# Kernel optimization log

Measured on AMD Instinct MI355X. Metric: run time of the kernel, lower is better.

The kernel has to match this reference:

```python
import jax, jax.numpy as jnp
import numpy as np

D = 1024; H = 8; QLR = 384; KVLR = 256; NOPE = 128; ROPE = 64; VD = 128
E = 8; TOPK = 2; INTER = 512; NSH = 2; B = 2; T = 2048
QKD = NOPE + ROPE  # 192


def _rms(x, w, eps=1e-6):
    return x * jax.lax.rsqrt(jnp.mean(x * x, axis=-1, keepdims=True) + eps) * w


def _rope(x, cos, sin):
    # x: [B,T,h,ROPE]; pairs are consecutive elements (torch view(...,-1,2)).
    x0 = x[..., 0::2]
    x1 = x[..., 1::2]
    c = cos[None, :, None, :]
    s = sin[None, :, None, :]
    y0 = x0 * c - x1 * s
    y1 = x0 * s + x1 * c
    return jnp.stack([y0, y1], axis=-1).reshape(x.shape)


def setup_inputs() -> dict:
    key = jax.random.key(0)
    ks = jax.random.split(key, 12)
    def w(k, shape, scale=0.02):
        return jax.random.normal(k, shape, dtype=jnp.float32) * scale
    inv = 1.0 / (10000.0 ** (jnp.arange(0, ROPE, 2, dtype=jnp.float32) / ROPE))
    ang = jnp.arange(T, dtype=jnp.float32)[:, None] * inv[None, :]  # [T, ROPE//2]
    return {
        "x": jax.random.normal(ks[0], (B, T, D), dtype=jnp.float32),
        "freqs_cos": jnp.cos(ang),
        "freqs_sin": jnp.sin(ang),
        "rmsn1_w": jnp.ones((D,), jnp.float32),
        "rmsn2_w": jnp.ones((D,), jnp.float32),
        "latent_w": w(ks[1], (D, QLR + KVLR + ROPE)),
        "q_norm_w": jnp.ones((QLR,), jnp.float32),
        "q_up_w": w(ks[2], (QLR, H * QKD)),
        "kv_norm_w": jnp.ones((KVLR,), jnp.float32),
        "kv_up_w": w(ks[3], (KVLR, H * (NOPE + VD))),
        "c_proj_w": w(ks[4], (D, D)),
        "gate_w": w(ks[5], (D, E)),
        "sh_w1": w(ks[6], (D, INTER * NSH)),
        "sh_w2": w(ks[7], (INTER * NSH, D)),
        "sh_w3": w(ks[8], (D, INTER * NSH)),
        "e_w1": w(ks[9], (E, D, INTER)),
        "e_w2": w(ks[10], (E, INTER, D)),
        "e_w3": w(ks[11], (E, D, INTER)),
    }


def reference(x, freqs_cos, freqs_sin, rmsn1_w, rmsn2_w, latent_w, q_norm_w,
              q_up_w, kv_norm_w, kv_up_w, c_proj_w, gate_w, sh_w1, sh_w2,
              sh_w3, e_w1, e_w2, e_w3):
    Bx, Tx, _ = x.shape
    # ---- MLA attention ----
    h = _rms(x, rmsn1_w)
    lat = h @ latent_w
    q_l, kv_l, k_r = jnp.split(lat, [QLR, QLR + KVLR], axis=-1)
    q = (_rms(q_l, q_norm_w) @ q_up_w).reshape(Bx, Tx, H, QKD)
    q_n, q_r = q[..., :NOPE], q[..., NOPE:]
    q_r = _rope(q_r, freqs_cos, freqs_sin)
    q = jnp.concatenate([q_n, q_r], axis=-1)  # [B,T,H,QKD]
    kv = (_rms(kv_l, kv_norm_w) @ kv_up_w).reshape(Bx, Tx, H, NOPE + VD)
    k_n, v = kv[..., :NOPE], kv[..., NOPE:]
    k_r = _rope(k_r[:, :, None, :], freqs_cos, freqs_sin)
    k_r = jnp.broadcast_to(k_r, (Bx, Tx, H, ROPE))
    k = jnp.concatenate([k_n, k_r], axis=-1)
    scale = 1.0 / jnp.sqrt(jnp.float32(QKD))
    scores = jnp.einsum('bqhd,bkhd->bhqk', q, k) * scale
    causal = jnp.tril(jnp.ones((Tx, Tx), dtype=bool))
    scores = jnp.where(causal, scores, jnp.finfo(scores.dtype).min)
    attn = jax.nn.softmax(scores, axis=-1)
    y = jnp.einsum('bhqk,bkhd->bqhd', attn, v).reshape(Bx, Tx, D)
    x = x + y @ c_proj_w
    # ---- DeepSeekMoE ----
    h2 = _rms(x, rmsn2_w).reshape(-1, D)  # [N, D]
    y_sh = (jax.nn.silu(h2 @ sh_w1) * (h2 @ sh_w3)) @ sh_w2
    scores_g = jax.nn.softmax(h2 @ gate_w, axis=-1)  # [N, E]
    w_top, idx = jax.lax.top_k(scores_g, TOPK)  # weights == gathered original scores
    # combine weights per expert (route_scale = 1.0)
    cw = jnp.sum(jax.nn.one_hot(idx, E, dtype=h2.dtype) * w_top[..., None], axis=1)  # [N, E]
    h1 = jnp.einsum('nd,edi->eni', h2, e_w1)
    h3 = jnp.einsum('nd,edi->eni', h2, e_w3)
    out_e = jnp.einsum('eni,eid->end', jax.nn.silu(h1) * h3, e_w2)  # [E, N, D]
    y_moe = y_sh + jnp.einsum('end,ne->nd', out_e, cw)
    return x + y_moe.reshape(Bx, Tx, D)
```

## Files before the change

kernel.cpp:

```cpp
#include <hip/hip_runtime.h>
#include <hip/hip_bf16.h>
#include <math.h>

#define D_ 1024
#define H_ 8
#define QLR_ 384
#define KVLR_ 256
#define NOPE_ 128
#define ROPE_ 64
#define VD_ 128
#define E_ 8
#define INTER_ 512
#define B_ 2
#define T_ 2048
#define QKD_ 192
#define NTOK (B_*T_)
#define LSTR 4608
#define MAXMB 72
#define NCH 40

typedef __attribute__((ext_vector_type(8))) short short8;
typedef __attribute__((ext_vector_type(4))) float f32x4;
typedef __attribute__((ext_vector_type(4))) unsigned short us4;

__device__ __forceinline__ unsigned short f2bf(float f) {
  union { float f; unsigned u; } v; v.f = f;
  return (unsigned short)((v.u + 0x7FFFu + ((v.u >> 16) & 1u)) >> 16);
}
__device__ __forceinline__ float bf2f(unsigned short h) {
  union { unsigned u; float f; } v; v.u = ((unsigned)h) << 16;
  return v.f;
}

#define GLD16(SRC, DST) __builtin_amdgcn_global_load_lds( \
    (__attribute__((address_space(1))) void*)(SRC), \
    (__attribute__((address_space(3))) void*)(DST), 16, 0, 0)

#define DPPF(v, ctrl) __int_as_float(__builtin_amdgcn_update_dpp(0, __float_as_int(v), ctrl, 0xF, 0xF, true))
__device__ __forceinline__ float dppmax16(float v) {
  v = fmaxf(v, DPPF(v, 0xB1));
  v = fmaxf(v, DPPF(v, 0x4E));
  v = fmaxf(v, DPPF(v, 0x124));
  v = fmaxf(v, DPPF(v, 0x128));
  return v;
}
__device__ __forceinline__ float dppsum16(float v) {
  v += DPPF(v, 0xB1);
  v += DPPF(v, 0x4E);
  v += DPPF(v, 0x124);
  v += DPPF(v, 0x128);
  return v;
}

__device__ __forceinline__ void trans32(const float* __restrict__ src, unsigned short* __restrict__ dst,
                                        int R, int C, int c0, int r0, float (*tile)[33]) {
  int tx = threadIdx.x & 31, ty = threadIdx.x >> 5;
  #pragma unroll
  for (int i = 0; i < 4; ++i) {
    int rr = ty + i * 8;
    tile[rr][tx] = src[(size_t)(r0 + rr) * C + c0 + tx];
  }
  __syncthreads();
  #pragma unroll
  for (int i = 0; i < 4; ++i) {
    int rr = ty + i * 8;
    dst[(size_t)(c0 + rr) * R + r0 + tx] = f2bf(tile[tx][rr]);
  }
}
__device__ __forceinline__ void trans32p(const float* __restrict__ src, unsigned short* __restrict__ dst,
                                         int K, int C1, int c0, int r0, int f, float (*tile)[33]) {
  int tx = threadIdx.x & 31, ty = threadIdx.x >> 5;
  #pragma unroll
  for (int i = 0; i < 4; ++i) {
    int rr = ty + i * 8;
    tile[rr][tx] = src[(size_t)(r0 + rr) * C1 + c0 + tx];
  }
  __syncthreads();
  #pragma unroll
  for (int i = 0; i < 4; ++i) {
    int cc = ty + i * 8;
    int c = c0 + cc;
    int n = ((c >> 4) << 5) + (c & 15) + f;
    dst[(size_t)n * K + r0 + tx] = f2bf(tile[tx][cc]);
  }
}

__global__ __launch_bounds__(256) void prep1(
    const float* __restrict__ x, const float* __restrict__ rw, unsigned short* __restrict__ h_bf,
    const float* __restrict__ latent_w, unsigned short* __restrict__ Wlat) {
  __shared__ float tile[32][33];
  int b = blockIdx.x;
  if (b < NTOK) {
    int tid = threadIdx.x;
    const float* xr = x + (size_t)b * D_;
    float v[4]; float ss = 0.f;
    #pragma unroll
    for (int j = 0; j < 4; ++j) { v[j] = xr[tid + j * 256]; ss += v[j] * v[j]; }
    for (int o = 1; o < 64; o <<= 1) ss += __shfl_xor(ss, o);
    if ((tid & 63) == 0) tile[32][tid >> 6] = ss;
    __syncthreads();
    float inv = 1.f / sqrtf((tile[32][0] + tile[32][1] + tile[32][2] + tile[32][3]) / D_ + 1e-6f);
    #pragma unroll
    for (int j = 0; j < 4; ++j) {
      int i = tid + j * 256;
      h_bf[(size_t)b * D_ + i] = f2bf(v[j] * inv * rw[i]);
    }
    return;
  }
  b -= NTOK;
  trans32(latent_w, Wlat, 1024, 704, (b % 22) * 32, (b / 22) * 32, tile);
}

__global__ __launch_bounds__(256) void prep2(
    const unsigned short* __restrict__ h_bf, const unsigned short* __restrict__ Wlat,
    unsigned short* __restrict__ lat,
    const float* __restrict__ q_up_w, unsigned short* __restrict__ Wqup,
    const float* __restrict__ kv_up_w, unsigned short* __restrict__ Wkv,
    const float* __restrict__ c_proj_w, unsigned short* __restrict__ Wcp,
    const float* __restrict__ sh_w1, const float* __restrict__ sh_w3, unsigned short* __restrict__ Wsh13,
    const float* __restrict__ sh_w2, unsigned short* __restrict__ Wsh2,
    const float* __restrict__ e_w1, const float* __restrict__ e_w3, unsigned short* __restrict__ Wew13,
    const float* __restrict__ e_w2, unsigned short* __restrict__ Wew2) {
  __shared__ __align__(16) unsigned short As[128 * 32];
  __shared__ __align__(16) unsigned short Bs[128 * 32];
  __shared__ float tile[32][33];
  int b = blockIdx.x;
  if (b < 192) {
    const int tid = threadIdx.x, lane = tid & 63, wave = tid >> 6;
    const int wm = wave >> 1, wn = wave & 1;
    const int bm = (b / 6) * 128, bn = (b % 6) * 128;
    const int r = lane & 15, g = lane >> 4;
    f32x4 acc[4][4];
    #pragma unroll
    for (int i = 0; i < 4; ++i)
      #pragma unroll
      for (int j = 0; j < 4; ++j) acc[i][j] = (f32x4)0.f;
    const int rl0 = wave * 16 + (lane >> 2), rl1 = rl0 + 64;
    const int kc = (lane & 3) * 8;
    char* AsB = (char*)As; char* BsB = (char*)Bs;
    for (int k0 = 0; k0 < 1024; k0 += 32) {
      GLD16(h_bf + (size_t)(bm + rl0) * 1024 + k0 + kc, AsB + wave * 1024);
      GLD16(h_bf + (size_t)(bm + rl1) * 1024 + k0 + kc, AsB + (wave + 4) * 1024);
      GLD16(Wlat + (size_t)(bn + rl0) * 1024 + k0 + kc, BsB + wave * 1024);
      GLD16(Wlat + (size_t)(bn + rl1) * 1024 + k0 + kc, BsB + (wave + 4) * 1024);
      __syncthreads();
      short8 af[4], bfr[4];
      #pragma unroll
      for (int mi = 0; mi < 4; ++mi)
        af[mi] = *(const short8*)(As + (wm * 64 + mi * 16 + r) * 32 + g * 8);
      #pragma unroll
      for (int nj = 0; nj < 4; ++nj)
        bfr[nj] = *(const short8*)(Bs + (wn * 64 + nj * 16 + r) * 32 + g * 8);
      #pragma unroll
      for (int mi = 0; mi < 4; ++mi)
        #pragma unroll
        for (int nj = 0; nj < 4; ++nj)
          acc[mi][nj] = __builtin_amdgcn_mfma_f32_16x16x32_bf16(af[mi], bfr[nj], acc[mi][nj], 0, 0, 0);
      __syncthreads();
    }
    const int orow0 = wm * 64 + g * 4;
    const int ocol0 = bn + wn * 64 + r;
    #pragma unroll
    for (int mi = 0; mi < 4; ++mi)
      #pragma unroll
      for (int reg = 0; reg < 4; ++reg) {
        int mrow = bm + orow0 + mi * 16 + reg;
        size_t bas = (size_t)mrow * 768 + ocol0;
        #pragma unroll
        for (int nj = 0; nj < 4; ++nj) lat[bas + nj * 16] = f2bf(acc[mi][nj][reg]);
      }
    return;
  }
  b -= 192;
  if (b < 576) { trans32(q_up_w, Wqup, 384, 1536, (b % 48) * 32, (b / 48) * 32, tile); return; }
  b -= 576;
  if (b < 512) { trans32(kv_up_w, Wkv, 256, 2048, (b % 64) * 32, (b / 64) * 32, tile); return; }
  b -= 512;
  if (b < 1024) { trans32(c_proj_w, Wcp, 1024, 1024, (b % 32) * 32, (b / 32) * 32, tile); return; }
  b -= 1024;
  if (b < 1024) { trans32(sh_w2, Wsh2, 1024, 1024, (b % 32) * 32, (b / 32) * 32, tile); return; }
  b -= 1024;
  if (b < 2048) {
    int z = b / 1024, idx = b % 1024;
    trans32p(z ? sh_w3 : sh_w1, Wsh13, 1024, 1024, (idx % 32) * 32, (idx / 32) * 32, z * 16, tile);
    return;
  }
  b -= 2048;
  if (b < 8192) {
    int z = b / 512, idx = b % 512;
    int bat = z >> 1, f = (z & 1) * 16;
    const float* src = ((z & 1) ? e_w3 : e_w1) + (size_t)bat * 1024 * 512;
    trans32p(src, Wew13 + (size_t)bat * 1024 * 1024, 1024, 512, (idx % 16) * 32, (idx / 16) * 32, f, tile);
    return;
  }
  b -= 8192;
  {
    int z = b / 512, idx = b % 512;
    trans32(e_w2 + (size_t)z * 512 * 1024, Wew2 + (size_t)z * 1024 * 512,
            512, 1024, (idx % 32) * 32, (idx / 32) * 32, tile);
  }
}

__global__ __launch_bounds__(256) void lat_post(
    const unsigned short* __restrict__ lat, const float* __restrict__ qw,
    const float* __restrict__ kw, const float* __restrict__ fc, const float* __restrict__ fs,
    unsigned short* __restrict__ qn, unsigned short* __restrict__ kvn,
    unsigned short* __restrict__ kr) {
  int row = blockIdx.x, tid = threadIdx.x;
  int lane = tid & 63, wv = tid >> 6;
  const unsigned short* lr = lat + (size_t)row * 768;
  float s1 = 0.f, s2 = 0.f;
  for (int i = tid; i < QLR_; i += 256) { float v = bf2f(lr[i]); s1 += v * v; }
  { float v = bf2f(lr[QLR_ + tid]); s2 = v * v; }
  for (int o = 1; o < 64; o <<= 1) { s1 += __shfl_xor(s1, o); s2 += __shfl_xor(s2, o); }
  __shared__ float red[8];
  if (lane == 0) { red[wv] = s1; red[4 + wv] = s2; }
  __syncthreads();
  float inv1 = 1.f / sqrtf((red[0] + red[1] + red[2] + red[3]) / QLR_ + 1e-6f);
  float inv2 = 1.f / sqrtf((red[4] + red[5] + red[6] + red[7]) / KVLR_ + 1e-6f);
  for (int i = tid; i < QLR_; i += 256)
    qn[(size_t)row * QLR_ + i] = f2bf(bf2f(lr[i]) * inv1 * qw[i]);
  kvn[(size_t)row * KVLR_ + tid] = f2bf(bf2f(lr[QLR_ + tid]) * inv2 * kw[tid]);
  if (tid < 32) {
    int t = row & (T_ - 1);
    float c = fc[t * 32 + tid], s = fs[t * 32 + tid];
    float x0 = bf2f(lr[640 + 2 * tid]), x1 = bf2f(lr[640 + 2 * tid + 1]);
    kr[(size_t)row * ROPE_ + 2 * tid]     = f2bf(x0 * c - x1 * s);
    kr[(size_t)row * ROPE_ + 2 * tid + 1] = f2bf(x0 * s + x1 * c);
  }
}

template<int MODE>
__global__ __launch_bounds__(256) void gemm_bf16(
    const unsigned short* __restrict__ A, const unsigned short* __restrict__ Bt,
    void* __restrict__ Cv, int M, int N, int K,
    const float* __restrict__ addv) {
  __shared__ __align__(16) unsigned short As[128 * 32];
  __shared__ __align__(16) unsigned short Bs[128 * 32];
  const int tid = threadIdx.x;
  const int lane = tid & 63, wave = tid >> 6;
  const int wm = wave >> 1, wn = wave & 1;
  const int bm = blockIdx.y * 128, bn = blockIdx.x * 128;
  const int r = lane & 15, g = lane >> 4;

  f32x4 acc[4][4];
  #pragma unroll
  for (int i = 0; i < 4; ++i)
    #pragma unroll
    for (int j = 0; j < 4; ++j) acc[i][j] = (f32x4)0.f;

  const int rl0 = wave * 16 + (lane >> 2);
  const int rl1 = rl0 + 64;
  const int kc = (lane & 3) * 8;
  char* AsB = (char*)As; char* BsB = (char*)Bs;

  for (int k0 = 0; k0 < K; k0 += 32) {
    GLD16(A + (size_t)(bm + rl0) * K + k0 + kc, AsB + wave * 1024);
    GLD16(A + (size_t)(bm + rl1) * K + k0 + kc, AsB + (wave + 4) * 1024);
    GLD16(Bt + (size_t)(bn + rl0) * K + k0 + kc, BsB + wave * 1024);
    GLD16(Bt + (size_t)(bn + rl1) * K + k0 + kc, BsB + (wave + 4) * 1024);
    __syncthreads();
    short8 af[4], bfr[4];
    #pragma unroll
    for (int mi = 0; mi < 4; ++mi)
      af[mi] = *(const short8*)(As + (wm * 64 + mi * 16 + r) * 32 + g * 8);
    #pragma unroll
    for (int nj = 0; nj < 4; ++nj)
      bfr[nj] = *(const short8*)(Bs + (wn * 64 + nj * 16 + r) * 32 + g * 8);
    #pragma unroll
    for (int mi = 0; mi < 4; ++mi)
      #pragma unroll
      for (int nj = 0; nj < 4; ++nj)
        acc[mi][nj] = __builtin_amdgcn_mfma_f32_16x16x32_bf16(af[mi], bfr[nj], acc[mi][nj], 0, 0, 0);
    __syncthreads();
  }

  const int orow0 = wm * 64 + g * 4;
  const int ocol0 = bn + wn * 64 + r;
  #pragma unroll
  for (int mi = 0; mi < 4; ++mi) {
    #pragma unroll
    for (int reg = 0; reg < 4; ++reg) {
      int mrow = bm + orow0 + mi * 16 + reg;
      size_t bas = (size_t)mrow * N + ocol0;
      if (MODE == 0) {
        unsigned short* C = (unsigned short*)Cv;
        #pragma unroll
        for (int nj = 0; nj < 4; ++nj) C[bas + nj * 16] = f2bf(acc[mi][nj][reg]);
      } else {
        float* C = (float*)Cv;
        #pragma unroll
        for (int nj = 0; nj < 4; ++nj) C[bas + nj * 16] = acc[mi][nj][reg] + addv[bas + nj * 16];
      }
    }
  }
}

__global__ __launch_bounds__(256) void gemm_qkv(
    const unsigned short* __restrict__ qn, const unsigned short* __restrict__ Wqup,
    const unsigned short* __restrict__ kvn, const unsigned short* __restrict__ Wkv,
    unsigned short* __restrict__ qq, unsigned short* __restrict__ kvb,
    unsigned short* __restrict__ vtg) {
  __shared__ __align__(16) unsigned short As[128 * 32];
  __shared__ __align__(16) unsigned short Bs[128 * 32];
  const int tid = threadIdx.x;
  const int lane = tid & 63, wave = tid >> 6;
  const int wm = wave >> 1, wn = wave & 1;
  const bool isQ = blockIdx.x < 12;
  const int bx = isQ ? blockIdx.x : blockIdx.x - 12;
  const unsigned short* A  = isQ ? qn : kvn;
  const unsigned short* Bt = isQ ? Wqup : Wkv;
  const int K = isQ ? QLR_ : KVLR_;
  const int bm = blockIdx.y * 128, bn = bx * 128;
  const int r = lane & 15, g = lane >> 4;

  f32x4 acc[4][4];
  #pragma unroll
  for (int i = 0; i < 4; ++i)
    #pragma unroll
    for (int j = 0; j < 4; ++j) acc[i][j] = (f32x4)0.f;

  const int rl0 = wave * 16 + (lane >> 2);
  const int rl1 = rl0 + 64;
  const int kc = (lane & 3) * 8;
  char* AsB = (char*)As; char* BsB = (char*)Bs;

  for (int k0 = 0; k0 < K; k0 += 32) {
    GLD16(A + (size_t)(bm + rl0) * K + k0 + kc, AsB + wave * 1024);
    GLD16(A + (size_t)(bm + rl1) * K + k0 + kc, AsB + (wave + 4) * 1024);
    GLD16(Bt + (size_t)(bn + rl0) * K + k0 + kc, BsB + wave * 1024);
    GLD16(Bt + (size_t)(bn + rl1) * K + k0 + kc, BsB + (wave + 4) * 1024);
    __syncthreads();
    short8 af[4], bfr[4];
    #pragma unroll
    for (int mi = 0; mi < 4; ++mi)
      af[mi] = *(const short8*)(As + (wm * 64 + mi * 16 + r) * 32 + g * 8);
    #pragma unroll
    for (int nj = 0; nj < 4; ++nj)
      bfr[nj] = *(const short8*)(Bs + (wn * 64 + nj * 16 + r) * 32 + g * 8);
    #pragma unroll
    for (int mi = 0; mi < 4; ++mi)
      #pragma unroll
      for (int nj = 0; nj < 4; ++nj)
        acc[mi][nj] = __builtin_amdgcn_mfma_f32_16x16x32_bf16(af[mi], bfr[nj], acc[mi][nj], 0, 0, 0);
    __syncthreads();
  }

  if (isQ) {
// ... 176 lines not shown

  for (int k0 = 0; k0 < K; k0 += 32) {
    GLD16(A + (size_t)(bm + rl0) * K + k0 + kc, AsB + wave * 1024);
    GLD16(A + (size_t)(bm + rl1) * K + k0 + kc, AsB + (wave + 4) * 1024);
    GLD16(Bt + (size_t)(bn + rl0) * K + k0 + kc, BsB + wave * 1024);
    GLD16(Bt + (size_t)(bn + rl1) * K + k0 + kc, BsB + (wave + 4) * 1024);
    __syncthreads();
    short8 af[4], bfr[4];
    #pragma unroll
    for (int mi = 0; mi < 4; ++mi)
      af[mi] = *(const short8*)(As + (wm * 64 + mi * 16 + r) * 32 + g * 8);
    #pragma unroll
    for (int nj = 0; nj < 4; ++nj)
      bfr[nj] = *(const short8*)(Bs + (wn * 64 + nj * 16 + r) * 32 + g * 8);
    #pragma unroll
    for (int mi = 0; mi < 4; ++mi)
      #pragma unroll
      for (int nj = 0; nj < 4; ++nj)
        acc[mi][nj] = __builtin_amdgcn_mfma_f32_16x16x32_bf16(af[mi], bfr[nj], acc[mi][nj], 0, 0, 0);
    __syncthreads();
  }

  const int ocol0 = bn + wn * 64 + r;
  if (isSh) {
    #pragma unroll
    for (int mi = 0; mi < 4; ++mi)
      #pragma unroll
      for (int reg = 0; reg < 4; ++reg) {
        int mrow = bm + wm * 64 + mi * 16 + g * 4 + reg;
        #pragma unroll
        for (int nj = 0; nj < 4; ++nj)
          atomicAdd(out + (size_t)mrow * 1024 + ocol0 + nj * 16, acc[mi][nj][reg]);
      }
  } else {
    #pragma unroll
    for (int mi = 0; mi < 4; ++mi)
      #pragma unroll
      for (int reg = 0; reg < 4; ++reg) {
        int orow = wm * 64 + mi * 16 + g * 4 + reg;
        int tok = lists[e * LSTR + ib * 128 + orow];
        if (tok >= 0) {
          float wt = cw[(size_t)tok * E_ + e];
          #pragma unroll
          for (int nj = 0; nj < 4; ++nj)
            atomicAdd(out + (size_t)tok * 1024 + ocol0 + nj * 16, acc[mi][nj][reg] * wt);
        }
      }
  }
}

#define AQ 128
#define AK 32
#define VP 40
__global__ __launch_bounds__(512) void attn_mfma(
    const unsigned short* __restrict__ q,
    const unsigned short* __restrict__ kv,
    const unsigned short* __restrict__ kr,
    const unsigned short* __restrict__ vt,
    const float* __restrict__ fcos, const float* __restrict__ fsin,
    unsigned short* __restrict__ po,
    float* __restrict__ pml) {
  __shared__ __align__(16) unsigned short Ks[AK * 192];
  __shared__ __align__(16) unsigned short Vl[128 * VP];
  __shared__ __align__(16) unsigned short Ps[8 * 16 * VP];
  const int tid = threadIdx.x, lane = tid & 63, wave = tid >> 6;
  const int r = lane & 15, g = lane >> 4;
  const int bh = blockIdx.y, b = bh >> 3, h = bh & 7;
  const int Stab[17] = {0,1,2,3,4,6,8,10,12,15,18,21,24,28,32,36,40};
  const int cid = (NCH - 1) - (int)blockIdx.x;
  int qt = 0;
  #pragma unroll
  for (int t = 1; t <= 15; ++t) if (cid >= Stab[t]) qt = t;
  const int chunk = cid - Stab[qt];
  const int q0 = qt * AQ;
  const int ntl = 4 * (qt + 1);
  const int kb = chunk * 16;
  const int ke = (kb + 16 < ntl) ? kb + 16 : ntl;
  const size_t bT = (size_t)b * T_;
  const unsigned short* vbase = vt + (size_t)bh * 64 * 4096;
  char* KsB = (char*)Ks;

  short8 qf[6];
  const int qrow = q0 + wave * 16 + r;
  {
    const unsigned short* qb = q + ((bT + qrow) * H_ + h) * 192;
    #pragma unroll
    for (int kk = 0; kk < 6; ++kk) qf[kk] = *(const short8*)(qb + kk * 32 + g * 8);
    #pragma unroll
    for (int kk = 4; kk < 6; ++kk) {
      int i0 = (kk - 4) * 16 + g * 4;
      #pragma unroll
      for (int p = 0; p < 4; ++p) {
        float cc = fcos[qrow * 32 + i0 + p], sn = fsin[qrow * 32 + i0 + p];
        float x0 = bf2f((unsigned short)qf[kk][2 * p]), x1 = bf2f((unsigned short)qf[kk][2 * p + 1]);
        qf[kk][2 * p]     = (short)f2bf(x0 * cc - x1 * sn);
        qf[kk][2 * p + 1] = (short)f2bf(x0 * sn + x1 * cc);
      }
    }
  }

  float m_i[4], l_i[4];
  f32x4 o[8];
  #pragma unroll
  for (int i = 0; i < 4; ++i) { m_i[i] = -1e30f; l_i[i] = 0.f; }
  #pragma unroll
  for (int cb = 0; cb < 8; ++cb) o[cb] = (f32x4)0.f;

  const float scale2 = 0.07216878364870322f * 1.44269504088896f;

  const int kr0r = tid / 24, kr0c = tid % 24;
  const bool k1v = tid < 256;
  const int kr1r = (tid + 512) / 24, kr1c = (tid + 512) % 24;

  short8 kreg0, kreg1, vreg;
  {
    int kk0 = kb * AK;
    kreg0 = (kr0c < 16)
      ? *(const short8*)(kv + ((bT + kk0 + kr0r) * H_ + h) * 128 + kr0c * 8)
      : *(const short8*)(kr + (bT + kk0 + kr0r) * 64 + (kr0c - 16) * 8);
    if (k1v)
      kreg1 = (kr1c < 16)
        ? *(const short8*)(kv + ((bT + kk0 + kr1r) * H_ + h) * 128 + kr1c * 8)
        : *(const short8*)(kr + (bT + kk0 + kr1r) * 64 + (kr1c - 16) * 8);
    vreg = *(const short8*)(vbase + (size_t)kb * 4096 + tid * 8);
  }

  for (int kt = kb; kt < ke; ++kt) {
    __builtin_amdgcn_s_barrier();
    __builtin_amdgcn_sched_barrier(0);
    *(short8*)(KsB + ((kr0r * 384 + kr0c * 16) ^ ((kr0r & 7) << 4))) = kreg0;
    if (k1v)
      *(short8*)(KsB + ((kr1r * 384 + kr1c * 16) ^ ((kr1r & 7) << 4))) = kreg1;
    *(short8*)(Vl + (tid >> 2) * VP + (tid & 3) * 8) = vreg;
// ... 36 lines not shown
      float s0 = sf0[reg] * scale2;
      float s1 = sf1[reg] * scale2;
      if (bnd) {
        int qp = q0 + wave * 16 + g * 4 + reg;
        if (k0 + r > qp) s0 = -1e30f;
        if (k0 + 16 + r > qp) s1 = -1e30f;
      }
      float mt = dppmax16(fmaxf(s0, s1));
      float fc = 1.f, mn = m_i[reg];
      if (mt > mn + 8.f) {
        mn = mt; fc = exp2f(m_i[reg] - mn); m_i[reg] = mn; needs = true;
      }
      float e0 = exp2f(s0 - mn), e1 = exp2f(s1 - mn);
      float rs = dppsum16(e0 + e1);
      l_i[reg] = l_i[reg] * fc + rs;
      fac[reg] = fc;
      __hip_bfloat162 pk = __float22bfloat162_rn(float2{e0, e1});
      unsigned u = *(unsigned*)&pk;
      int prow = g * 4 + reg;
      Ps[wave * 16 * VP + prow * VP + r] = (unsigned short)u;
      Ps[wave * 16 * VP + prow * VP + 16 + r] = (unsigned short)(u >> 16);
    }
    if (__any(needs)) {
      #pragma unroll
      for (int cb = 0; cb < 8; ++cb)
        #pragma unroll
        for (int reg = 0; reg < 4; ++reg) o[cb][reg] *= fac[reg];
    }
    short8 pa = *(const short8*)(Ps + wave * 16 * VP + r * VP + g * 8);
    __builtin_amdgcn_s_setprio(1);
    #pragma unroll
    for (int cb = 0; cb < 8; ++cb) {
      short8 vb = *(const short8*)(Vl + (cb * 16 + r) * VP + g * 8);
      o[cb] = __builtin_amdgcn_mfma_f32_16x16x32_bf16(pa, vb, o[cb], 0, 0, 0);
    }
    __builtin_amdgcn_s_setprio(0);
  }

  const int slab = bh * NCH + cid;
  unsigned short* pob = po + (size_t)slab * 16384;
  float* pmlb = pml + (size_t)slab * 256;
  #pragma unroll
  for (int reg = 0; reg < 4; ++reg) {
    int row = wave * 16 + g * 4 + reg;
    if (r == 0) { pmlb[row * 2] = m_i[reg]; pmlb[row * 2 + 1] = l_i[reg]; }
    #pragma unroll
    for (int cb = 0; cb < 8; ++cb)
      pob[row * 128 + cb * 16 + r] = f2bf(o[cb][reg]);
  }
}

__global__ __launch_bounds__(512) void attn_combine(
    const unsigned short* __restrict__ po, const float* __restrict__ pml,
    unsigned short* __restrict__ y) {
  const int qt = blockIdx.x, bh = blockIdx.y, b = bh >> 3, h = bh & 7;
  const int Stab[17] = {0,1,2,3,4,6,8,10,12,15,18,21,24,28,32,36,40};
  const int s0 = bh * NCH + Stab[qt];
  const int nc = Stab[qt + 1] - Stab[qt];
  const int row = threadIdx.x >> 2;
  const int qp = threadIdx.x & 3;
  float mj[4], lj[4], ej[4];
  float m = -1e30f;
  #pragma unroll
  for (int j = 0; j < 4; ++j) {
    if (j < nc) {
      mj[j] = pml[(size_t)(s0 + j) * 256 + row * 2];
      lj[j] = pml[(size_t)(s0 + j) * 256 + row * 2 + 1];
      m = fmaxf(m, mj[j]);
    }
  }
  float lsum = 0.f;
  #pragma unroll
  for (int j = 0; j < 4; ++j) {
    if (j < nc) {
      ej[j] = exp2f(mj[j] - m);
      lsum += lj[j] * ej[j];
    }
  }
  float inv = 1.f / lsum;
  unsigned short* yb = y + ((size_t)(b * T_ + qt * 128 + row)) * 1024 + h * 128 + qp * 32;
  #pragma unroll
  for (int v = 0; v < 4; ++v) {
    float accv[8];
    #pragma unroll
    for (int jj = 0; jj < 8; ++jj) accv[jj] = 0.f;
    #pragma unroll
    for (int j = 0; j < 4; ++j) {
      if (j < nc) {
        const unsigned short* oj = po + (size_t)(s0 + j) * 16384 + row * 128 + qp * 32 + v * 8;
        short8 a = *(const short8*)oj;
        float w = ej[j];
        #pragma unroll
        for (int jj = 0; jj < 8; ++jj) accv[jj] += bf2f((unsigned short)a[jj]) * w;
      }
    }
    short8 wv;
    #pragma unroll
    for (int jj = 0; jj < 8; ++jj) wv[jj] = (short)f2bf(accv[jj] * inv);
    *(short8*)(yb + v * 8) = wv;
  }
}

__global__ __launch_bounds__(256) void rms2_gate(
    const float* __restrict__ xo, const float* __restrict__ rw, const float* __restrict__ gw,
    unsigned short* __restrict__ h2b, float* __restrict__ cw, int* __restrict__ done) {
  int row = blockIdx.x, tid = threadIdx.x;
  int lane = tid & 63, wv = tid >> 6;
  if (row == 0 && tid == 0) *done = 0;
  const float* xr = xo + (size_t)row * D_;
  float v[4]; float ss = 0.f;
  #pragma unroll
  for (int j = 0; j < 4; ++j) { v[j] = xr[tid + j * 256]; ss += v[j] * v[j]; }
  for (int o = 1; o < 64; o <<= 1) ss += __shfl_xor(ss, o);
  __shared__ float red[4];
  if (lane == 0) red[wv] = ss;
  __syncthreads();
  float inv = 1.f / sqrtf((red[0] + red[1] + red[2] + red[3]) / D_ + 1e-6f);
  float a[E_] = {0, 0, 0, 0, 0, 0, 0, 0};
  #pragma unroll
  for (int j = 0; j < 4; ++j) {
    int i = tid + j * 256;
    float hv = v[j] * inv * rw[i];
    h2b[(size_t)row * D_ + i] = f2bf(hv);
    const float* wr = gw + (size_t)i * E_;
    #pragma unroll
    for (int e = 0; e < E_; ++e) a[e] += hv * wr[e];
  }
  #pragma unroll
  for (int e = 0; e < E_; ++e) {
    float t = a[e];
    for (int o = 1; o < 64; o <<= 1) t += __shfl_xor(t, o);
    a[e] = t;
  }
// ... 85 lines not shown
  const float* kv_norm_w= (const float*)d_in[8];
  const float* kv_up_w  = (const float*)d_in[9];
  const float* c_proj_w = (const float*)d_in[10];
  const float* gate_w   = (const float*)d_in[11];
  const float* sh_w1    = (const float*)d_in[12];
  const float* sh_w2    = (const float*)d_in[13];
  const float* sh_w3    = (const float*)d_in[14];
  const float* e_w1     = (const float*)d_in[15];
  const float* e_w2     = (const float*)d_in[16];
  const float* e_w3     = (const float*)d_in[17];
  float* out = (float*)d_out;

  char* base = (char*)d_ws;
  size_t off = 0;
  auto take = [&](size_t bytes) { char* p = base + off; off += (bytes + 255) & ~(size_t)255; return p; };
  unsigned short* Wlat  = (unsigned short*)take((size_t)768 * 1024 * 2);
  unsigned short* Wqup  = (unsigned short*)take((size_t)1536 * 384 * 2);
  unsigned short* Wkv   = (unsigned short*)take((size_t)2048 * 256 * 2);
  unsigned short* Wcp   = (unsigned short*)take((size_t)1024 * 1024 * 2);
  unsigned short* Wsh13 = (unsigned short*)take((size_t)2048 * 1024 * 2);
  unsigned short* Wsh2  = (unsigned short*)take((size_t)1024 * 1024 * 2);
  unsigned short* Wew13 = (unsigned short*)take((size_t)8 * 1024 * 1024 * 2);
  unsigned short* Wew2  = (unsigned short*)take((size_t)8 * 1024 * 512 * 2);
  float* cw             = (float*)take((size_t)NTOK * E_ * 4);
  int* lists            = (int*)take((size_t)E_ * LSTR * 4);
  int* counts           = (int*)take(64 * 4);
  int* map              = (int*)take(MAXMB * 4);
  int* sbase            = (int*)take(E_ * 4);
  int* done             = (int*)take(64 * 4);
  unsigned short* Vtg   = (unsigned short*)take((size_t)16 * 64 * 4096 * 2);
  unsigned short* kr    = (unsigned short*)take((size_t)NTOK * 64 * 2);

  size_t actStart = off;
  size_t aoff = actStart;
  auto takeA = [&](size_t bytes) { char* p = base + aoff; aoff += (bytes + 255) & ~(size_t)255; return p; };
  unsigned short* h_bf = (unsigned short*)takeA((size_t)NTOK * 1024 * 2);
  unsigned short* lat  = (unsigned short*)takeA((size_t)NTOK * 768 * 2);
  unsigned short* qn   = (unsigned short*)takeA((size_t)NTOK * 384 * 2);
  unsigned short* kvn  = (unsigned short*)takeA((size_t)NTOK * 256 * 2);
  unsigned short* qq   = (unsigned short*)takeA((size_t)NTOK * 1536 * 2);
  unsigned short* kvb  = (unsigned short*)takeA((size_t)NTOK * 1024 * 2);
  unsigned short* y    = (unsigned short*)takeA((size_t)NTOK * 1024 * 2);
  unsigned short* po   = (unsigned short*)takeA((size_t)16 * NCH * 16384 * 2);
  float* pml           = (float*)takeA((size_t)16 * NCH * 256 * 4);

  size_t coff = actStart;
  auto takeC = [&](size_t bytes) { char* p = base + coff; coff += (bytes + 255) & ~(size_t)255; return p; };
  unsigned short* h2b  = (unsigned short*)takeC((size_t)NTOK * 1024 * 2);
  unsigned short* t1m  = (unsigned short*)takeC((size_t)NTOK * 1024 * 2);
  unsigned short* ehm  = (unsigned short*)takeC((size_t)9216 * 512 * 2);

  dim3 blk(256);

  prep1<<<dim3(NTOK + 704), blk, 0, stream>>>(x, rmsn1_w, h_bf, latent_w, Wlat);
  prep2<<<dim3(192 + 576 + 512 + 1024 + 1024 + 2048 + 8192 + 4096), blk, 0, stream>>>(
      h_bf, Wlat, lat, q_up_w, Wqup, kv_up_w, Wkv, c_proj_w, Wcp,
      sh_w1, sh_w3, Wsh13, sh_w2, Wsh2, e_w1, e_w3, Wew13, e_w2, Wew2);
  lat_post<<<NTOK, blk, 0, stream>>>(lat, q_norm_w, kv_norm_w, fcos, fsin, qn, kvn, kr);
  gemm_qkv<<<dim3(28, 32), blk, 0, stream>>>(qn, Wqup, kvn, Wkv, qq, kvb, Vtg);
  attn_mfma<<<dim3(NCH, 16), dim3(512), 0, stream>>>(qq, kvb, kr, Vtg, fcos, fsin, po, pml);
  attn_combine<<<dim3(16, 16), dim3(512), 0, stream>>>(po, pml, y);
  gemm_bf16<1><<<dim3(8, 32), blk, 0, stream>>>(y, Wcp, out, NTOK, 1024, 1024, x);
  rms2_gate<<<NTOK, blk, 0, stream>>>(out, rmsn2_w, gate_w, h2b, cw, done);
  moe_build<<<E_, blk, 0, stream>>>(cw, lists, counts, map, sbase, done);
  gemm_ffn13<<<dim3(1088), blk, 0, stream>>>(h2b, Wsh13, t1m, Wew13, ehm, lists, map, sbase);
  gemm_ffn2<<<dim3(832), blk, 0, stream>>>(t1m, Wsh2, ehm, Wew2, out, lists, map, sbase, cw);
}
```

Before: 345.6 us.

## Overlap late-stage weight transposes with attention by merging into one grid

```diff
diff --git a/kernel.cpp b/kernel.cpp
--- a/kernel.cpp
+++ b/kernel.cpp
@@ -52,9 +52,9 @@
   return v;
 }
 
-__device__ __forceinline__ void trans32(const float* __restrict__ src, unsigned short* __restrict__ dst,
-                                        int R, int C, int c0, int r0, float (*tile)[33]) {
-  int tx = threadIdx.x & 31, ty = threadIdx.x >> 5;
+__device__ __forceinline__ void htrans32(const float* __restrict__ src, unsigned short* __restrict__ dst,
+                                         int R, int C, int c0, int r0, float (*tile)[33], int tid) {
+  int tx = tid & 31, ty = tid >> 5;
   #pragma unroll
   for (int i = 0; i < 4; ++i) {
     int rr = ty + i * 8;
@@ -67,9 +67,9 @@
     dst[(size_t)(c0 + rr) * R + r0 + tx] = f2bf(tile[tx][rr]);
   }
 }
-__device__ __forceinline__ void trans32p(const float* __restrict__ src, unsigned short* __restrict__ dst,
-                                         int K, int C1, int c0, int r0, int f, float (*tile)[33]) {
-  int tx = threadIdx.x & 31, ty = threadIdx.x >> 5;
+__device__ __forceinline__ void htrans32p(const float* __restrict__ src, unsigned short* __restrict__ dst,
+                                          int K, int C1, int c0, int r0, int f, float (*tile)[33], int tid) {
+  int tx = tid & 31, ty = tid >> 5;
   #pragma unroll
   for (int i = 0; i < 4; ++i) {
     int rr = ty + i * 8;
@@ -88,7 +88,7 @@
 __global__ __launch_bounds__(256) void prep1(
     const float* __restrict__ x, const float* __restrict__ rw, unsigned short* __restrict__ h_bf,
     const float* __restrict__ latent_w, unsigned short* __restrict__ Wlat) {
-  __shared__ float tile[32][33];
+  __shared__ float tile[33][33];
   int b = blockIdx.x;
   if (b < NTOK) {
     int tid = threadIdx.x;
@@ -108,19 +108,14 @@
     return;
   }
   b -= NTOK;
-  trans32(latent_w, Wlat, 1024, 704, (b % 22) * 32, (b / 22) * 32, tile);
+  htrans32(latent_w, Wlat, 1024, 704, (b % 22) * 32, (b / 22) * 32, (float(*)[33])tile, threadIdx.x);
 }
 
 __global__ __launch_bounds__(256) void prep2(
     const unsigned short* __restrict__ h_bf, const unsigned short* __restrict__ Wlat,
     unsigned short* __restrict__ lat,
     const float* __restrict__ q_up_w, unsigned short* __restrict__ Wqup,
-    const float* __restrict__ kv_up_w, unsigned short* __restrict__ Wkv,
-    const float* __restrict__ c_proj_w, unsigned short* __restrict__ Wcp,
-    const float* __restrict__ sh_w1, const float* __restrict__ sh_w3, unsigned short* __restrict__ Wsh13,
-    const float* __restrict__ sh_w2, unsigned short* __restrict__ Wsh2,
-    const float* __restrict__ e_w1, const float* __restrict__ e_w3, unsigned short* __restrict__ Wew13,
-    const float* __restrict__ e_w2, unsigned short* __restrict__ Wew2) {
+    const float* __restrict__ kv_up_w, unsigned short* __restrict__ Wkv) {
   __shared__ __align__(16) unsigned short As[128 * 32];
   __shared__ __align__(16) unsigned short Bs[128 * 32];
   __shared__ float tile[32][33];
@@ -172,33 +167,9 @@
     return;
   }
   b -= 192;
-  if (b < 576) { trans32(q_up_w, Wqup, 384, 1536, (b % 48) * 32, (b / 48) * 32, tile); return; }
+  if (b < 576) { htrans32(q_up_w, Wqup, 384, 1536, (b % 48) * 32, (b / 48) * 32, tile, threadIdx.x); return; }
   b -= 576;
-  if (b < 512) { trans32(kv_up_w, Wkv, 256, 2048, (b % 64) * 32, (b / 64) * 32, tile); return; }
-  b -= 512;
-  if (b < 1024) { trans32(c_proj_w, Wcp, 1024, 1024, (b % 32) * 32, (b / 32) * 32, tile); return; }
-  b -= 1024;
-  if (b < 1024) { trans32(sh_w2, Wsh2, 1024, 1024, (b % 32) * 32, (b / 32) * 32, tile); return; }
-  b -= 1024;
-  if (b < 2048) {
-    int z = b / 1024, idx = b % 1024;
-    trans32p(z ? sh_w3 : sh_w1, Wsh13, 1024, 1024, (idx % 32) * 32, (idx / 32) * 32, z * 16, tile);
-    return;
-  }
-  b -= 2048;
-  if (b < 8192) {
-    int z = b / 512, idx = b % 512;
-    int bat = z >> 1, f = (z & 1) * 16;
-    const float* src = ((z & 1) ? e_w3 : e_w1) + (size_t)bat * 1024 * 512;
-    trans32p(src, Wew13 + (size_t)bat * 1024 * 1024, 1024, 512, (idx % 16) * 32, (idx / 16) * 32, f, tile);
-    return;
-  }
-  b -= 8192;
-  {
-    int z = b / 512, idx = b % 512;
-    trans32(e_w2 + (size_t)z * 512 * 1024, Wew2 + (size_t)z * 1024 * 512,
-            512, 1024, (idx % 32) * 32, (idx / 32) * 32, tile);
-  }
+  htrans32(kv_up_w, Wkv, 256, 2048, (b % 64) * 32, (b / 64) * 32, tile, threadIdx.x);
 }
 
 __global__ __launch_bounds__(256) void lat_post(
@@ -576,22 +547,62 @@
 #define AQ 128
 #define AK 32
 #define VP 40
-__global__ __launch_bounds__(512) void attn_mfma(
+__global__ __launch_bounds__(512) void attn_plus(
     const unsigned short* __restrict__ q,
     const unsigned short* __restrict__ kv,
     const unsigned short* __restrict__ kr,
     const unsigned short* __restrict__ vt,
     const float* __restrict__ fcos, const float* __restrict__ fsin,
     unsigned short* __restrict__ po,
-    float* __restrict__ pml) {
+    float* __restrict__ pml,
+    const float* __restrict__ c_proj_w, unsigned short* __restrict__ Wcp,
+    const float* __restrict__ sh_w1, const float* __restrict__ sh_w3, unsigned short* __restrict__ Wsh13,
+    const float* __restrict__ sh_w2, unsigned short* __restrict__ Wsh2,
+    const float* __restrict__ e_w1, const float* __restrict__ e_w3, unsigned short* __restrict__ Wew13,
+    const float* __restrict__ e_w2, unsigned short* __restrict__ Wew2) {
   __shared__ __align__(16) unsigned short Ks[AK * 192];
   __shared__ __align__(16) unsigned short Vl[128 * VP];
   __shared__ __align__(16) unsigned short Ps[8 * 16 * VP];
+  char* KsB = (char*)Ks;
+
+  if (blockIdx.x >= 640) {
+    int sub = threadIdx.x >> 8;
+    int tid = threadIdx.x & 255;
+    float (*tile)[33] = (float(*)[33])(KsB + sub * 4224);
+    int t = ((int)blockIdx.x - 640) * 2 + sub;
+    if (t < 1024) { htrans32(c_proj_w, Wcp, 1024, 1024, (t % 32) * 32, (t / 32) * 32, tile, tid); return; }
+    t -= 1024;
+    if (t < 1024) { htrans32(sh_w2, Wsh2, 1024, 1024, (t % 32) * 32, (t / 32) * 32, tile, tid); return; }
+    t -= 1024;
+    if (t < 2048) {
+      int z = t / 1024, idx = t % 1024;
+      htrans32p(z ? sh_w3 : sh_w1, Wsh13, 1024, 1024, (idx % 32) * 32, (idx / 32) * 32, z * 16, tile, tid);
+      return;
+    }
+    t -= 2048;
+    if (t < 8192) {
+      int z = t / 512, idx = t % 512;
+      int bat = z >> 1, f = (z & 1) * 16;
+      const float* src = ((z & 1) ? e_w3 : e_w1) + (size_t)bat * 1024 * 512;
+      htrans32p(src, Wew13 + (size_t)bat * 1024 * 1024, 1024, 512, (idx % 16) * 32, (idx / 16) * 32, f, tile, tid);
+      return;
+    }
+    t -= 8192;
+    {
+      int z = t / 512, idx = t % 512;
+      htrans32(e_w2 + (size_t)z * 512 * 1024, Wew2 + (size_t)z * 1024 * 512,
+               512, 1024, (idx % 32) * 32, (idx / 32) * 32, tile, tid);
+    }
+    return;
+  }
+
+  const int ab = blockIdx.x;
+  const int cidx = ab >> 4;
+  const int bh = ab & 15, b = bh >> 3, h = bh & 7;
   const int tid = threadIdx.x, lane = tid & 63, wave = tid >> 6;
   const int r = lane & 15, g = lane >> 4;
-  const int bh = blockIdx.y, b = bh >> 3, h = bh & 7;
   const int Stab[17] = {0,1,2,3,4,6,8,10,12,15,18,21,24,28,32,36,40};
-  const int cid = (NCH - 1) - (int)blockIdx.x;
+  const int cid = (NCH - 1) - cidx;
   int qt = 0;
   #pragma unroll
   for (int t = 1; t <= 15; ++t) if (cid >= Stab[t]) qt = t;
@@ -602,7 +613,6 @@
   const int ke = (kb + 16 < ntl) ? kb + 16 : ntl;
   const size_t bT = (size_t)b * T_;
   const unsigned short* vbase = vt + (size_t)bh * 64 * 4096;
-  char* KsB = (char*)Ks;
 
   short8 qf[6];
   const int qrow = q0 + wave * 16 + r;
@@ -964,12 +974,12 @@
   dim3 blk(256);
 
   prep1<<<dim3(NTOK + 704), blk, 0, stream>>>(x, rmsn1_w, h_bf, latent_w, Wlat);
-  prep2<<<dim3(192 + 576 + 512 + 1024 + 1024 + 2048 + 8192 + 4096), blk, 0, stream>>>(
-      h_bf, Wlat, lat, q_up_w, Wqup, kv_up_w, Wkv, c_proj_w, Wcp,
-      sh_w1, sh_w3, Wsh13, sh_w2, Wsh2, e_w1, e_w3, Wew13, e_w2, Wew2);
+  prep2<<<dim3(192 + 576 + 512), blk, 0, stream>>>(h_bf, Wlat, lat, q_up_w, Wqup, kv_up_w, Wkv);
   lat_post<<<NTOK, blk, 0, stream>>>(lat, q_norm_w, kv_norm_w, fcos, fsin, qn, kvn, kr);
   gemm_qkv<<<dim3(28, 32), blk, 0, stream>>>(qn, Wqup, kvn, Wkv, qq, kvb, Vtg);
-  attn_mfma<<<dim3(NCH, 16), dim3(512), 0, stream>>>(qq, kvb, kr, Vtg, fcos, fsin, po, pml);
+  attn_plus<<<dim3(640 + 8192), dim3(512), 0, stream>>>(
+      qq, kvb, kr, Vtg, fcos, fsin, po, pml,
+      c_proj_w, Wcp, sh_w1, sh_w3, Wsh13, sh_w2, Wsh2, e_w1, e_w3, Wew13, e_w2, Wew2);
   attn_combine<<<dim3(16, 16), dim3(512), 0, stream>>>(po, pml, y);
   gemm_bf16<1><<<dim3(8, 32), blk, 0, stream>>>(y, Wcp, out, NTOK, 1024, 1024, x);
   rms2_gate<<<NTOK, blk, 0, stream>>>(out, rmsn2_w, gate_w, h2b, cw, done);
```

After: 346.4 us. No clear change (+0.2%).

## Batch weight transposes per block, move q/kv transposes to prep1, split-K c_proj

Applied to the files above, without the earlier changes.

```diff
diff --git a/kernel.cpp b/kernel.cpp
--- a/kernel.cpp
+++ b/kernel.cpp
@@ -52,9 +52,10 @@
   return v;
 }
 
-__device__ __forceinline__ void trans32(const float* __restrict__ src, unsigned short* __restrict__ dst,
-                                        int R, int C, int c0, int r0, float (*tile)[33]) {
-  int tx = threadIdx.x & 31, ty = threadIdx.x >> 5;
+__device__ __forceinline__ void htrans32(const float* __restrict__ src, unsigned short* __restrict__ dst,
+                                         int R, int C, int c0, int r0, float (*tile)[33], int tid) {
+  int tx = tid & 31, ty = tid >> 5;
+  __syncthreads();
   #pragma unroll
   for (int i = 0; i < 4; ++i) {
     int rr = ty + i * 8;
@@ -67,9 +68,10 @@
     dst[(size_t)(c0 + rr) * R + r0 + tx] = f2bf(tile[tx][rr]);
   }
 }
-__device__ __forceinline__ void trans32p(const float* __restrict__ src, unsigned short* __restrict__ dst,
-                                         int K, int C1, int c0, int r0, int f, float (*tile)[33]) {
-  int tx = threadIdx.x & 31, ty = threadIdx.x >> 5;
+__device__ __forceinline__ void htrans32p(const float* __restrict__ src, unsigned short* __restrict__ dst,
+                                          int K, int C1, int c0, int r0, int f, float (*tile)[33], int tid) {
+  int tx = tid & 31, ty = tid >> 5;
+  __syncthreads();
   #pragma unroll
   for (int i = 0; i < 4; ++i) {
     int rr = ty + i * 8;
@@ -87,11 +89,13 @@
 
 __global__ __launch_bounds__(256) void prep1(
     const float* __restrict__ x, const float* __restrict__ rw, unsigned short* __restrict__ h_bf,
-    const float* __restrict__ latent_w, unsigned short* __restrict__ Wlat) {
-  __shared__ float tile[32][33];
+    const float* __restrict__ latent_w, unsigned short* __restrict__ Wlat,
+    const float* __restrict__ q_up_w, unsigned short* __restrict__ Wqup,
+    const float* __restrict__ kv_up_w, unsigned short* __restrict__ Wkv) {
+  __shared__ float tile[33][33];
   int b = blockIdx.x;
+  int tid = threadIdx.x;
   if (b < NTOK) {
-    int tid = threadIdx.x;
     const float* xr = x + (size_t)b * D_;
     float v[4]; float ss = 0.f;
     #pragma unroll
@@ -108,14 +112,32 @@
     return;
   }
   b -= NTOK;
-  trans32(latent_w, Wlat, 1024, 704, (b % 22) * 32, (b / 22) * 32, tile);
+  float (*tp)[33] = (float(*)[33])tile;
+  if (b < 176) {
+    for (int j = 0; j < 4; ++j) {
+      int t = b * 4 + j;
+      htrans32(latent_w, Wlat, 1024, 704, (t % 22) * 32, (t / 22) * 32, tp, tid);
+    }
+    return;
+  }
+  b -= 176;
+  if (b < 144) {
+    for (int j = 0; j < 4; ++j) {
+      int t = b * 4 + j;
+      htrans32(q_up_w, Wqup, 384, 1536, (t % 48) * 32, (t / 48) * 32, tp, tid);
+    }
+    return;
+  }
+  b -= 144;
+  for (int j = 0; j < 4; ++j) {
+    int t = b * 4 + j;
+    htrans32(kv_up_w, Wkv, 256, 2048, (t % 64) * 32, (t / 64) * 32, tp, tid);
+  }
 }
 
 __global__ __launch_bounds__(256) void prep2(
     const unsigned short* __restrict__ h_bf, const unsigned short* __restrict__ Wlat,
     unsigned short* __restrict__ lat,
-    const float* __restrict__ q_up_w, unsigned short* __restrict__ Wqup,
-    const float* __restrict__ kv_up_w, unsigned short* __restrict__ Wkv,
     const float* __restrict__ c_proj_w, unsigned short* __restrict__ Wcp,
     const float* __restrict__ sh_w1, const float* __restrict__ sh_w3, unsigned short* __restrict__ Wsh13,
     const float* __restrict__ sh_w2, unsigned short* __restrict__ Wsh2,
@@ -125,8 +147,9 @@
   __shared__ __align__(16) unsigned short Bs[128 * 32];
   __shared__ float tile[32][33];
   int b = blockIdx.x;
+  int tid = threadIdx.x;
   if (b < 192) {
-    const int tid = threadIdx.x, lane = tid & 63, wave = tid >> 6;
+    const int lane = tid & 63, wave = tid >> 6;
     const int wm = wave >> 1, wn = wave & 1;
     const int bm = (b / 6) * 128, bn = (b % 6) * 128;
     const int r = lane & 15, g = lane >> 4;
@@ -172,32 +195,55 @@
     return;
   }
   b -= 192;
-  if (b < 576) { trans32(q_up_w, Wqup, 384, 1536, (b % 48) * 32, (b / 48) * 32, tile); return; }
-  b -= 576;
-  if (b < 512) { trans32(kv_up_w, Wkv, 256, 2048, (b % 64) * 32, (b / 64) * 32, tile); return; }
+  float (*tp)[33] = (float(*)[33])tile;
+  if (b < 256) {
+    for (int j = 0; j < 4; ++j) {
+      int t = b * 4 + j;
+      htrans32(c_proj_w, Wcp, 1024, 1024, (t % 32) * 32, (t / 32) * 32, tp, tid);
+    }
+    return;
+  }
+  b -= 256;
+  if (b < 256) {
+    for (int j = 0; j < 4; ++j) {
+      int t = b * 4 + j;
+      htrans32(sh_w2, Wsh2, 1024, 1024, (t % 32) * 32, (t / 32) * 32, tp, tid);
+    }
+    return;
+  }
+  b -= 256;
+  if (b < 512) {
+    int t0 = b * 4;
+    int z = t0 / 1024;
+    const float* src = z ? sh_w3 : sh_w1;
+    for (int j = 0; j < 4; ++j) {
+      int idx = (t0 + j) % 1024;
+      htrans32p(src, Wsh13, 1024, 1024, (idx % 32) * 32, (idx / 32) * 32, z * 16, tp, tid);
+    }
+    return;
+  }
   b -= 512;
-  if (b < 1024) { trans32(c_proj_w, Wcp, 1024, 1024, (b % 32) * 32, (b / 32) * 32, tile); return; }
-  b -= 1024;
-  if (b < 1024) { trans32(sh_w2, Wsh2, 1024, 1024, (b % 32) * 32, (b / 32) * 32, tile); return; }
-  b -= 1024;
   if (b < 2048) {
-    int z = b / 1024, idx = b % 1024;
-    trans32p(z ? sh_w3 : sh_w1, Wsh13, 1024, 1024, (idx % 32) * 32, (idx / 32) * 32, z * 16, tile);
+    int t0 = b * 4;
+    int z = t0 / 512, bat = z >> 1, f = (z & 1) * 16;
+    const float* src = ((z & 1) ? e_w3 : e_w1) + (size_t)bat * 1024 * 512;
+    unsigned short* dst = Wew13 + (size_t)bat * 1024 * 1024;
+    for (int j = 0; j < 4; ++j) {
+      int idx = (t0 + j) % 512;
+      htrans32p(src, dst, 1024, 512, (idx % 16) * 32, (idx / 16) * 32, f, tp, tid);
+    }
     return;
   }
   b -= 2048;
-  if (b < 8192) {
-    int z = b / 512, idx = b % 512;
-    int bat = z >> 1, f = (z & 1) * 16;
-    const float* src = ((z & 1) ? e_w3 : e_w1) + (size_t)bat * 1024 * 512;
-    trans32p(src, Wew13 + (size_t)bat * 1024 * 1024, 1024, 512, (idx % 16) * 32, (idx / 16) * 32, f, tile);
-    return;
-  }
-  b -= 8192;
   {
-    int z = b / 512, idx = b % 512;
-    trans32(e_w2 + (size_t)z * 512 * 1024, Wew2 + (size_t)z * 1024 * 512,
-            512, 1024, (idx % 32) * 32, (idx / 32) * 32, tile);
+    int t0 = b * 4;
+    int z = t0 / 512;
+    const float* src = e_w2 + (size_t)z * 512 * 1024;
+    unsigned short* dst = Wew2 + (size_t)z * 1024 * 512;
+    for (int j = 0; j < 4; ++j) {
+      int idx = (t0 + j) % 512;
+      htrans32(src, dst, 512, 1024, (idx % 32) * 32, (idx / 32) * 32, tp, tid);
+    }
   }
 }
 
@@ -230,17 +276,16 @@
   }
 }
 
-template<int MODE>
-__global__ __launch_bounds__(256) void gemm_bf16(
+__global__ __launch_bounds__(256) void gemm_cproj(
     const unsigned short* __restrict__ A, const unsigned short* __restrict__ Bt,
-    void* __restrict__ Cv, int M, int N, int K,
-    const float* __restrict__ addv) {
+    float* __restrict__ out) {
   __shared__ __align__(16) unsigned short As[128 * 32];
   __shared__ __align__(16) unsigned short Bs[128 * 32];
   const int tid = threadIdx.x;
   const int lane = tid & 63, wave = tid >> 6;
   const int wm = wave >> 1, wn = wave & 1;
   const int bm = blockIdx.y * 128, bn = blockIdx.x * 128;
+  const int koff = blockIdx.z * 512;
   const int r = lane & 15, g = lane >> 4;
 
   f32x4 acc[4][4];
@@ -254,11 +299,11 @@
   const int kc = (lane & 3) * 8;
   char* AsB = (char*)As; char* BsB = (char*)Bs;
 
-  for (int k0 = 0; k0 < K; k0 += 32) {
-    GLD16(A + (size_t)(bm + rl0) * K + k0 + kc, AsB + wave * 1024);
-    GLD16(A + (size_t)(bm + rl1) * K + k0 + kc, AsB + (wave + 4) * 1024);
-    GLD16(Bt + (size_t)(bn + rl0) * K + k0 + kc, BsB + wave * 1024);
-    GLD16(Bt + (size_t)(bn + rl1) * K + k0 + kc, BsB + (wave + 4) * 1024);
+  for (int k0 = 0; k0 < 512; k0 += 32) {
+    GLD16(A + (size_t)(bm + rl0) * 1024 + koff + k0 + kc, AsB + wave * 1024);
+    GLD16(A + (size_t)(bm + rl1) * 1024 + koff + k0 + kc, AsB + (wave + 4) * 1024);
+    GLD16(Bt + (size_t)(bn + rl0) * 1024 + koff + k0 + kc, BsB + wave * 1024);
+    GLD16(Bt + (size_t)(bn + rl1) * 1024 + koff + k0 + kc, BsB + (wave + 4) * 1024);
     __syncthreads();
     short8 af[4], bfr[4];
     #pragma unroll
@@ -278,22 +323,15 @@
   const int orow0 = wm * 64 + g * 4;
   const int ocol0 = bn + wn * 64 + r;
   #pragma unroll
-  for (int mi = 0; mi < 4; ++mi) {
+  for (int mi = 0; mi < 4; ++mi)
     #pragma unroll
     for (int reg = 0; reg < 4; ++reg) {
       int mrow = bm + orow0 + mi * 16 + reg;
-      size_t bas = (size_t)mrow * N + ocol0;
-      if (MODE == 0) {
-        unsigned short* C = (unsigned short*)Cv;
-        #pragma unroll
-        for (int nj = 0; nj < 4; ++nj) C[bas + nj * 16] = f2bf(acc[mi][nj][reg]);
-      } else {
-        float* C = (float*)Cv;
-        #pragma unroll
-        for (int nj = 0; nj < 4; ++nj) C[bas + nj * 16] = acc[mi][nj][reg] + addv[bas + nj * 16];
-      }
-    }
-  }
+      size_t bas = (size_t)mrow * 1024 + ocol0;
+      #pragma unroll
+      for (int nj = 0; nj < 4; ++nj)
+        atomicAdd(out + bas + nj * 16, acc[mi][nj][reg]);
+    }
 }
 
 __global__ __launch_bounds__(256) void gemm_qkv(
@@ -745,13 +783,21 @@
 
 __global__ __launch_bounds__(512) void attn_combine(
     const unsigned short* __restrict__ po, const float* __restrict__ pml,
-    unsigned short* __restrict__ y) {
+    unsigned short* __restrict__ y,
+    const float* __restrict__ x, float* __restrict__ out) {
   const int qt = blockIdx.x, bh = blockIdx.y, b = bh >> 3, h = bh & 7;
   const int Stab[17] = {0,1,2,3,4,6,8,10,12,15,18,21,24,28,32,36,40};
   const int s0 = bh * NCH + Stab[qt];
   const int nc = Stab[qt + 1] - Stab[qt];
   const int row = threadIdx.x >> 2;
   const int qp = threadIdx.x & 3;
+  const size_t grow = (size_t)(b * T_ + qt * 128 + row);
+  {
+    const float4* xs = (const float4*)(x + grow * 1024 + h * 128 + qp * 32);
+    float4* od = (float4*)(out + grow * 1024 + h * 128 + qp * 32);
+    #pragma unroll
+    for (int v2 = 0; v2 < 8; ++v2) od[v2] = xs[v2];
+  }
   float mj[4], lj[4], ej[4];
   float m = -1e30f;
   #pragma unroll
@@ -771,7 +817,7 @@
     }
   }
   float inv = 1.f / lsum;
-  unsigned short* yb = y + ((size_t)(b * T_ + qt * 128 + row)) * 1024 + h * 128 + qp * 32;
+  unsigned short* yb = y + grow * 1024 + h * 128 + qp * 32;
   #pragma unroll
   for (int v = 0; v < 4; ++v) {
     float accv[8];
@@ -963,15 +1009,15 @@
 
   dim3 blk(256);
 
-  prep1<<<dim3(NTOK + 704), blk, 0, stream>>>(x, rmsn1_w, h_bf, latent_w, Wlat);
-  prep2<<<dim3(192 + 576 + 512 + 1024 + 1024 + 2048 + 8192 + 4096), blk, 0, stream>>>(
-      h_bf, Wlat, lat, q_up_w, Wqup, kv_up_w, Wkv, c_proj_w, Wcp,
-      sh_w1, sh_w3, Wsh13, sh_w2, Wsh2, e_w1, e_w3, Wew13, e_w2, Wew2);
+  prep1<<<dim3(NTOK + 448), blk, 0, stream>>>(x, rmsn1_w, h_bf, latent_w, Wlat,
+                                              q_up_w, Wqup, kv_up_w, Wkv);
+  prep2<<<dim3(192 + 4096), blk, 0, stream>>>(h_bf, Wlat, lat,
+      c_proj_w, Wcp, sh_w1, sh_w3, Wsh13, sh_w2, Wsh2, e_w1, e_w3, Wew13, e_w2, Wew2);
   lat_post<<<NTOK, blk, 0, stream>>>(lat, q_norm_w, kv_norm_w, fcos, fsin, qn, kvn, kr);
   gemm_qkv<<<dim3(28, 32), blk, 0, stream>>>(qn, Wqup, kvn, Wkv, qq, kvb, Vtg);
   attn_mfma<<<dim3(NCH, 16), dim3(512), 0, stream>>>(qq, kvb, kr, Vtg, fcos, fsin, po, pml);
-  attn_combine<<<dim3(16, 16), dim3(512), 0, stream>>>(po, pml, y);
-  gemm_bf16<1><<<dim3(8, 32), blk, 0, stream>>>(y, Wcp, out, NTOK, 1024, 1024, x);
+  attn_combine<<<dim3(16, 16), dim3(512), 0, stream>>>(po, pml, y, x, out);
+  gemm_cproj<<<dim3(8, 32, 2), blk, 0, stream>>>(y, Wcp, out);
   rms2_gate<<<NTOK, blk, 0, stream>>>(out, rmsn2_w, gate_w, h2b, cw, done);
   moe_build<<<E_, blk, 0, stream>>>(cw, lists, counts, map, sbase, done);
   gemm_ffn13<<<dim3(1088), blk, 0, stream>>>(h2b, Wsh13, t1m, Wew13, ehm, lists, map, sbase);
```

Result: slower. 361.3 us (+4.5%).
